# Optimization experiments

Hardware: AMD Instinct MI355X
Metric: run time of the kernel (lower is better)

The kernel has to match this reference:

```python
import jax, jax.numpy as jnp
import numpy as np

N = 50000          # nodes
E = 800000         # edges
IN_F = 128         # in_features
C = 1.0            # curvature (all learnable curvatures init to 1.0)
GIN_EPS = 0.0      # LorentzGIN eps
EPS = 1e-7
NUM_CLASSES = 10


def arcosh(x):
    x = jnp.maximum(x, 1.0 + EPS)
    return jnp.log(x + jnp.sqrt(x * x - 1.0))


def log_map_zero(y, c):
    # log map at hyperboloid origin (sqrt(c),0,...,0); tangent with first coord 0
    sc = np.sqrt(c).astype(np.float32)
    y0, tail = y[..., :1], y[..., 1:]
    dist = sc * arcosh(y0 / sc + EPS)                       # induced distance to origin
    nrm = jnp.sqrt(jnp.sum(tail * tail, axis=-1, keepdims=True) + EPS)
    return jnp.concatenate([jnp.zeros_like(y0), dist / nrm * tail], axis=-1)


def exp_map_zero(dp, c):
    # exp map at origin; dp tangent with first coord 0; re-normalized onto hyperboloid
    sc = np.sqrt(c).astype(np.float32)
    tail = dp[..., 1:]
    n = jnp.sqrt(jnp.clip(jnp.sum(tail * tail, axis=-1, keepdims=True) + EPS, 1e-6, None))
    n_cut = jnp.minimum(n, 50.0)
    tail_out = sc * jnp.sinh(n_cut / sc) * tail / n
    first = jnp.sqrt(c + jnp.sum(tail_out * tail_out, axis=-1, keepdims=True))
    return jnp.concatenate([first, tail_out], axis=-1)


def lorentz_linear(x, W, b, c):
    # matvec_regular: log-map, affine map on spatial coords, exp-map back
    xt = log_map_zero(x, c)                                  # first coord is 0
    mx = jnp.concatenate([xt[..., :1], xt[..., 1:] @ W.T + b], axis=-1)
    h = exp_map_zero(mx, c)
    cond = jnp.all(mx == 0, axis=-1, keepdims=True)
    return jnp.where(cond, 0.0, h)


def lorentz_act(x, c_in, c_out, act):
    xt = act(log_map_zero(x, c_in))
    xt = xt.at[..., 0].set(0.0)                              # normalize_tangent_zero
    return exp_map_zero(xt, c_out)


def forward(x, edge_index, W0, b0, W1, b1, W2, b2, Wc, bc):
    # LorentzGIN: tangent-space GIN aggregation (1+eps)*x_t + sum_{j in N(i)} x_t[j]
    xt = log_map_zero(x, C)
    agg = jax.ops.segment_sum(xt[edge_index[0]], edge_index[1], num_segments=N)
    out = (1.0 + GIN_EPS) * xt + agg
    out = out.at[..., 0].set(0.0)
    h = exp_map_zero(out, C)
    for (W, b) in ((W0, b0), (W1, b1), (W2, b2)):
        h = lorentz_act(lorentz_linear(h, W, b, C), C, C, jax.nn.relu)
    # manifold mean pooling over nodes
    ht = log_map_zero(h, C)                                  # [N, 384]
    hm = jnp.mean(ht, axis=0)                                # [384]
    hm = hm.at[0].set(0.0)                                   # normalize_tangent_zero
    h_classify = lorentz_linear(hm, Wc, bc, C)               # [NUM_CLASSES]
    prob = lorentz_act(h_classify, C, C, lambda t: jax.nn.softmax(t, axis=-1))
    return h_classify, prob


def setup_inputs():
    key = jax.random.key(0)
    ks = jax.random.split(key, 6)
    tail = 0.5 * jax.random.normal(ks[0], (N, IN_F - 1), jnp.float32)
    x0 = jnp.sqrt(C + jnp.sum(tail * tail, axis=-1, keepdims=True))
    x = jnp.concatenate([x0, tail], axis=-1)                 # points on the hyperboloid
    edge_index = jax.random.randint(ks[1], (2, E), 0, N)

    def lin(k, o, i):
        kw, kb = jax.random.split(k)
        s = 1.0 / np.sqrt(i)
        return (jax.random.uniform(kw, (o - 1, i - 1), jnp.float32, -s, s),
                jax.random.uniform(kb, (o - 1,), jnp.float32, -s, s))

    W0, b0 = lin(ks[2], 128, 128)
    W1, b1 = lin(ks[3], 256, 128)
    W2, b2 = lin(ks[4], 384, 256)
    Wc, bc = lin(ks[5], NUM_CLASSES, 384)
    return dict(x=x, edge_index=edge_index, W0=W0, b0=b0, W1=W1, b1=b1,
                W2=W2, b2=b2, Wc=Wc, bc=bc)


def reference(x, edge_index, W0, b0, W1, b1, W2, b2, Wc, bc):
    return forward(x, edge_index, W0, b0, W1, b1, W2, b2, Wc, bc)
```

## Files before the change

### kernel.cpp

```cpp
#include <hip/hip_runtime.h>
#include <math.h>

#define EPSF 1e-7f

typedef unsigned short ushort_t;
typedef __attribute__((ext_vector_type(8))) short bf16x8;
typedef __attribute__((ext_vector_type(4))) float f32x4;

__device__ __forceinline__ float fsinh(float x) { return 0.5f * (__expf(x) - __expf(-x)); }
__device__ __forceinline__ float arcosh_f(float x) {
    x = fmaxf(x, 1.0f + EPSF);
    return __logf(x + sqrtf(x * x - 1.0f));
}

__device__ __forceinline__ unsigned short f2bf(float f) {
    union { float f; unsigned u; } c; c.f = f;
    unsigned r = c.u + 0x7FFFu + ((c.u >> 16) & 1u);
    return (unsigned short)(r >> 16);
}
__device__ __forceinline__ float bf2f(unsigned short u) {
    union { unsigned u; float f; } c; c.u = ((unsigned)u) << 16;
    return c.f;
}

__device__ __forceinline__ float wredsum(float v) {
#pragma unroll
    for (int off = 32; off; off >>= 1) v += __shfl_xor(v, off, 64);
    return v;
}

__device__ __forceinline__ float ep_coef(float s1, float sp) {
    bool allz = (s1 == 0.0f);
    float n1 = sqrtf(fmaxf(s1 + EPSF, 1e-6f));
    float fac1 = fsinh(fminf(n1, 50.f)) / n1;
    float S2 = allz ? 0.f : fac1 * fac1 * s1;
    float first1 = allz ? 0.f : sqrtf(1.f + S2);
    float dist = arcosh_f(first1 + EPSF);
    float rs = dist / sqrtf(S2 + EPSF);
    float coef1 = allz ? 0.f : rs * fac1;
    float S3 = coef1 * coef1 * sp;
    float n2 = sqrtf(fmaxf(S3 + EPSF, 1e-6f));
    float fac2 = fsinh(fminf(n2, 50.f)) / n2;
    float S4 = fac2 * fac2 * S3;
    float first2 = sqrtf(1.f + S4);
    float dist2 = arcosh_f(first2 + EPSF);
    return dist2 / sqrtf(S4 + EPSF) * fac2 * coef1;
}

__device__ __forceinline__ void llds16(const void* g, void* l) {
    __builtin_amdgcn_global_load_lds((const __attribute__((address_space(1))) unsigned int*)g,
                                     (__attribute__((address_space(3))) unsigned int*)l,
                                     16, 0, 0);
}

__global__ __launch_bounds__(64) void k_log0(const float* __restrict__ x,
                                             char* __restrict__ Abase, int N) {
    int i = blockIdx.x, t = threadIdx.x;
    float2 v = *reinterpret_cast<const float2*>(x + (size_t)i * 128 + 2 * t);
    float y0 = __shfl(v.x, 0, 64);
    float a0 = (t == 0) ? 0.f : v.x;
    float s = wredsum(a0 * a0 + v.y * v.y);
    float dist = arcosh_f(y0 + EPSF);
    float scl = dist / sqrtf(s + EPSF);
    ushort2 o;
    o.x = f2bf(scl * a0);
    o.y = f2bf(scl * v.y);
    *reinterpret_cast<ushort2*>(Abase + (size_t)i * 512 + 256 + 4 * t) = o;
}

__global__ __launch_bounds__(256) void k_c1(const int* __restrict__ edst,
                                            int* __restrict__ gcnt,
                                            int E, int NBKT, int EPB) {
    __shared__ int cnt[64];
    int blk = blockIdx.x, t = threadIdx.x;
    for (int i = t; i < NBKT; i += 256) cnt[i] = 0;
    __syncthreads();
    int lo = blk * EPB, hi = min(lo + EPB, E);
    for (int e = lo + t; e < hi; e += 256) atomicAdd(&cnt[edst[e] >> 10], 1);
    __syncthreads();
    for (int i = t; i < NBKT; i += 256) gcnt[blk * NBKT + i] = cnt[i];
}

__global__ __launch_bounds__(64) void k_c2(int* __restrict__ gcnt,
                                           int* __restrict__ bstart, int NBLK, int NBKT) {
    __shared__ int sh[10816];
    __shared__ int tot[64];
    __shared__ int bs[65];
    int t = threadIdx.x;
    int total = NBLK * NBKT;
    for (int i = t; i < total; i += 64) sh[i] = gcnt[i];
    __syncthreads();
    if (t < NBKT) {
        int run = 0;
        for (int blk = 0; blk < NBLK; ++blk) {
            int idx = blk * NBKT + t;
            int c = sh[idx]; sh[idx] = run; run += c;
        }
        tot[t] = run;
    }
    __syncthreads();
    if (t == 0) {
        int r = 0;
        for (int b = 0; b < NBKT; ++b) { bs[b] = r; r += tot[b]; }
        bs[NBKT] = r;
    }
    __syncthreads();
    if (t < NBKT) {
        bstart[t] = bs[t];
        if (t == 0) bstart[NBKT] = bs[NBKT];
    }
    for (int i = t; i < total; i += 64) gcnt[i] = sh[i] + bs[i % NBKT];
}

__global__ __launch_bounds__(256) void k_c3(const int* __restrict__ esrc,
                                            const int* __restrict__ edst,
                                            const int* __restrict__ gcnt,
                                            int* __restrict__ ebuf,
                                            int E, int NBKT, int EPB) {
    __shared__ int cur[64];
    int blk = blockIdx.x, t = threadIdx.x;
    for (int i = t; i < NBKT; i += 256) cur[i] = 0;
    __syncthreads();
    int lo = blk * EPB, hi = min(lo + EPB, E);
    for (int e = lo + t; e < hi; e += 256) {
        int d = edst[e], s = esrc[e];
        int b = d >> 10;
        int r = atomicAdd(&cur[b], 1);
        ebuf[gcnt[blk * NBKT + b] + r] = ((d & 1023) << 17) | s;
    }
}

__global__ __launch_bounds__(1024) void k_c4(const int* __restrict__ ebuf,
                                             const int* __restrict__ bstart,
                                             int* __restrict__ row_ptr,
                                             int* __restrict__ srcl,
                                             int N, int NBKT, int E) {
    __shared__ int cnt[1024];
    __shared__ int cur[1024];
    __shared__ int wsum[17];
    int b = blockIdx.x, t = threadIdx.x;
    int lane = t & 63, wv = t >> 6;
    int lo = b << 10;
    int nn = min(1024, N - lo);
    cnt[t] = 0;
    __syncthreads();
    int es = bstart[b], ee = bstart[b + 1];
    for (int e = es + t; e < ee; e += 1024) atomicAdd(&cnt[ebuf[e] >> 17], 1);
    __syncthreads();
    int c = cnt[t];
    int sc = c;
#pragma unroll
    for (int off = 1; off < 64; off <<= 1) {
        int v = __shfl_up(sc, off, 64);
        if (lane >= off) sc += v;
    }
    if (lane == 63) wsum[wv + 1] = sc;
    if (t == 0) wsum[0] = 0;
    __syncthreads();
    if (t == 0) {
        for (int w = 1; w < 16; ++w) wsum[w + 1] += wsum[w];
    }
    __syncthreads();
    int rp = es + wsum[wv] + sc - c;
    cur[t] = rp;
    if (t < nn) row_ptr[lo + t] = rp;
    if (b == NBKT - 1 && t == 0) row_ptr[N] = E;
    __syncthreads();
    for (int e = es + t; e < ee; e += 1024) {
        int p = ebuf[e];
        int r = atomicAdd(&cur[p >> 17], 1);
        srcl[r] = p & 0x1FFFF;
    }
}

__global__ __launch_bounds__(64) void k_agg(const char* __restrict__ Abase,
                                            const int* __restrict__ row_ptr,
                                            const int* __restrict__ srcl,
                                            ushort_t* __restrict__ Ab, int N) {
    int i = blockIdx.x, t = threadIdx.x;
    const char* base = Abase + 256 + 4 * t;
    ushort2 sv = *reinterpret_cast<const ushort2*>(base + (size_t)i * 512);
    float p0[8], p1[8];
    p0[0] = bf2f(sv.x); p1[0] = bf2f(sv.y);
#pragma unroll
    for (int q = 1; q < 8; ++q) { p0[q] = 0.f; p1[q] = 0.f; }
    int b = row_ptr[i], e = row_ptr[i + 1];
    int k = b;
    for (; k + 8 <= e; k += 8) {
        int s[8];
#pragma unroll
        for (int q = 0; q < 8; ++q) s[q] = srcl[k + q];
        ushort2 v[8];
#pragma unroll
        for (int q = 0; q < 8; ++q)
            v[q] = *reinterpret_cast<const ushort2*>(base + (size_t)s[q] * 512);
#pragma unroll
        for (int q = 0; q < 8; ++q) { p0[q] += bf2f(v[q].x); p1[q] += bf2f(v[q].y); }
    }
    for (; k < e; ++k) {
        int s = srcl[k];
        ushort2 v = *reinterpret_cast<const ushort2*>(base + (size_t)s * 512);
        p0[0] += bf2f(v.x); p1[0] += bf2f(v.y);
    }
    float u0 = ((p0[0] + p0[1]) + (p0[2] + p0[3])) + ((p0[4] + p0[5]) + (p0[6] + p0[7]));
    float u1 = ((p1[0] + p1[1]) + (p1[2] + p1[3])) + ((p1[4] + p1[5]) + (p1[6] + p1[7]));
    if (t == 0) u0 = 0.f;
    float s1 = wredsum(u0 * u0 + u1 * u1);
    float n = sqrtf(fmaxf(s1 + EPSF, 1e-6f));
    float fac = fsinh(fminf(n, 50.f)) / n;
    float S2 = fac * fac * s1;
    float first = sqrtf(1.f + S2);
    float dist = arcosh_f(first + EPSF);
    float C = dist / sqrtf(S2 + EPSF) * fac;
    ushort2 o;
    o.x = f2bf(C * u0);
    o.y = f2bf(C * u1);
    *reinterpret_cast<ushort2*>(Ab + (size_t)i * 256 + 2 * t) = o;
}

__global__ void k_convw3(const float* __restrict__ W0, const float* __restrict__ W1,
                         const float* __restrict__ W2,
                         ushort_t* __restrict__ Wb0, ushort_t* __restrict__ Wb1,
                         ushort_t* __restrict__ Wb2,
                         int o1, int i1, int Kp1, int o2, int i2, int Kp2,
                         int o3, int i3, int Kp3, int t1, int t2, int t3) {
    int idx = blockIdx.x * blockDim.x + threadIdx.x;
    const float* W; ushort_t* Wb; int ncols, K, Kp, shift;
    if (idx < t1) { W = W0; Wb = Wb0; ncols = o1; K = i1; Kp = Kp1; shift = 1; }
    else if (idx < t1 + t2) { idx -= t1; W = W1; Wb = Wb1; ncols = o2; K = i2; Kp = Kp2; shift = 0; }
    else if (idx < t1 + t2 + t3) { idx -= t1 + t2; W = W2; Wb = Wb2; ncols = o3; K = i3; Kp = Kp3; shift = 0; }
    else return;
    int o = idx / Kp, kk = idx - o * Kp;
    int ks = kk - shift;
    float v = 0.f;
    if (o < ncols && ks >= 0 && ks < K) v = W[(size_t)o * K + ks];
    Wb[idx] = f2bf(v);
}

__global__ __launch_bounds__(256) void k_gemm(const ushort_t* __restrict__ Ab, int lda,
                                              const ushort_t* __restrict__ Wb, int ldw,
                                              const float* __restrict__ bias,
                                              ushort_t* __restrict__ Yb, int ldy,
                                              int Kp, int ncols) {
    __shared__ ushort_t As[128 * 32];
    __shared__ ushort_t Bs[128 * 32];
    int tid = threadIdx.x;
    int lane = tid & 63, wv = tid >> 6;
    int bm = blockIdx.x * 128, bn = blockIdx.y * 128;
    int r = lane & 15, g4 = lane >> 4;
    int wr = (wv >> 1) * 64, wc = (wv & 1) * 64;

    f32x4 acc[4][4] = {};
    for (int k0 = 0; k0 < Kp; k0 += 32) {
#pragma unroll
        for (int ci = 0; ci < 2; ++ci) {
            int L = (wv * 2 + ci) * 1024 + lane * 16;
            int row = L >> 6, kb = L & 63;
            const char* ga = (const char*)Ab + ((size_t)(bm + row) * lda + k0) * 2 + kb;
            llds16(ga, (char*)As + (wv * 2 + ci) * 1024);
            const char* gb = (const char*)Wb + ((size_t)(bn + row) * ldw + k0) * 2 + kb;
            llds16(gb, (char*)Bs + (wv * 2 + ci) * 1024);
        }
        __syncthreads();
        bf16x8 af[4], bfr[4];
#pragma unroll
        for (int m = 0; m < 4; ++m)
            af[m] = *reinterpret_cast<const bf16x8*>((const char*)As + (wr + m * 16 + r) * 64 + g4 * 16);
#pragma unroll
        for (int n2 = 0; n2 < 4; ++n2)
            bfr[n2] = *reinterpret_cast<const bf16x8*>((const char*)Bs + (wc + n2 * 16 + r) * 64 + g4 * 16);
#pragma unroll
        for (int m = 0; m < 4; ++m)
#pragma unroll
            for (int n2 = 0; n2 < 4; ++n2)
                acc[m][n2] = __builtin_amdgcn_mfma_f32_16x16x32_bf16(af[m], bfr[n2], acc[m][n2], 0, 0, 0);
        __syncthreads();
    }
#pragma unroll
    for (int n2 = 0; n2 < 4; ++n2) {
        int col = bn + wc + n2 * 16 + r;
        if (col >= ncols) continue;
        float bv = bias[col];
#pragma unroll
        for (int m = 0; m < 4; ++m) {
#pragma unroll
            for (int j = 0; j < 4; ++j) {
                int row = bm + wr + m * 16 + g4 * 4 + j;
                Yb[(size_t)row * ldy + col] = f2bf(acc[m][n2][j] + bv);
            }
        }
    }
}

__global__ __launch_bounds__(256) void k_gemmf(const ushort_t* __restrict__ Ab, int lda,
                                               const ushort_t* __restrict__ Wb, int ldw,
                                               const float* __restrict__ bias,
                                               ushort_t* __restrict__ Out,
                                               int Kp, int ncols) {
    __shared__ ushort_t As[128 * 32];
    __shared__ ushort_t Bs[128 * 32];
    __shared__ float s1buf[2][128];
    __shared__ float spbuf[2][128];
    __shared__ float Cbuf[128];
    int tid = threadIdx.x;
    int lane = tid & 63, wv = tid >> 6;
    int bm = blockIdx.x * 128;
    int r = lane & 15, g4 = lane >> 4;
    int wr = (wv >> 1) * 64, wc = (wv & 1) * 64;
    int half = wv & 1;

    f32x4 acc[4][4] = {};
    for (int k0 = 0; k0 < Kp; k0 += 32) {
#pragma unroll
        for (int ci = 0; ci < 2; ++ci) {
            int L = (wv * 2 + ci) * 1024 + lane * 16;
            int row = L >> 6, kb = L & 63;
            const char* ga = (const char*)Ab + ((size_t)(bm + row) * lda + k0) * 2 + kb;
            llds16(ga, (char*)As + (wv * 2 + ci) * 1024);
            const char* gb = (const char*)Wb + ((size_t)(row) * ldw + k0) * 2 + kb;
            llds16(gb, (char*)Bs + (wv * 2 + ci) * 1024);
        }
        __syncthreads();
        bf16x8 af[4], bfr[4];
#pragma unroll
        for (int m = 0; m < 4; ++m)
            af[m] = *reinterpret_cast<const bf16x8*>((const char*)As + (wr + m * 16 + r) * 64 + g4 * 16);
#pragma unroll
        for (int n2 = 0; n2 < 4; ++n2)
            bfr[n2] = *reinterpret_cast<const bf16x8*>((const char*)Bs + (wc + n2 * 16 + r) * 64 + g4 * 16);
#pragma unroll
        for (int m = 0; m < 4; ++m)
#pragma unroll
            for (int n2 = 0; n2 < 4; ++n2)
                acc[m][n2] = __builtin_amdgcn_mfma_f32_16x16x32_bf16(af[m], bfr[n2], acc[m][n2], 0, 0, 0);
        __syncthreads();
    }
    float bv[4];
#pragma unroll
    for (int n2 = 0; n2 < 4; ++n2) {
        int col = wc + n2 * 16 + r;
        bv[n2] = (col < ncols) ? bias[col] : 0.f;
    }
#pragma unroll
    for (int m = 0; m < 4; ++m) {
#pragma unroll
        for (int j = 0; j < 4; ++j) {
            float s1l = 0.f, spl = 0.f;
#pragma unroll
            for (int n2 = 0; n2 < 4; ++n2) {
                int col = wc + n2 * 16 + r;
                float y = (col < ncols) ? (acc[m][n2][j] + bv[n2]) : 0.f;
                acc[m][n2][j] = y;
                s1l += y * y;
                float ym = fmaxf(y, 0.f);
                spl += ym * ym;
            }
#pragma unroll
            for (int off = 1; off < 16; off <<= 1) {
                s1l += __shfl_xor(s1l, off, 64);
                spl += __shfl_xor(spl, off, 64);
            }
            if (r == 0) {
                int row = wr + m * 16 + g4 * 4 + j;
                s1buf[half][row] = s1l;
                spbuf[half][row] = spl;
            }
        }
    }
    __syncthreads();
    if (tid < 128) {
        float s1 = s1buf[0][tid] + s1buf[1][tid];
        float sp = spbuf[0][tid] + spbuf[1][tid];
        Cbuf[tid] = ep_coef(s1, sp);
    }
    __syncthreads();
#pragma unroll
    for (int m = 0; m < 4; ++m) {
#pragma unroll
        for (int j = 0; j < 4; ++j) {
            int rloc = wr + m * 16 + g4 * 4 + j;
            float C = Cbuf[rloc];
            size_t rowoff = (size_t)(bm + rloc) * 256;
#pragma unroll
            for (int n2 = 0; n2 < 4; ++n2) {
                int col = wc + n2 * 16 + r;
                Out[rowoff + col] = f2bf(C * fmaxf(acc[m][n2][j], 0.f));
            }
        }
    }
}

template <int NCP>
__global__ __launch_bounds__(64) void k_ep(const ushort_t* __restrict__ Y, int ldy,
                                           ushort_t* __restrict__ out, int ldo, int N) {
    constexpr int CH = NCP / 128;
    int i = blockIdx.x, t = threadIdx.x;
    const ushort_t* yr = Y + (size_t)i * ldy;
    float y[2 * CH], ym[2 * CH];
#pragma unroll
    for (int c = 0; c < CH; ++c) {
        ushort2 v = *reinterpret_cast<const ushort2*>(yr + c * 128 + 2 * t);
        y[2 * c] = bf2f(v.x);
        y[2 * c + 1] = bf2f(v.y);
    }
    if (t == 63) y[2 * CH - 1] = 0.f;
    float s1l = 0.f, spl = 0.f;
#pragma unroll
    for (int q = 0; q < 2 * CH; ++q) {
        s1l += y[q] * y[q];
        ym[q] = fmaxf(y[q], 0.f);
        spl += ym[q] * ym[q];
    }
#pragma unroll
    for (int off = 32; off; off >>= 1) {
        s1l += __shfl_xor(s1l, off, 64);
        spl += __shfl_xor(spl, off, 64);
    }
    float C = ep_coef(s1l, spl);
    ushort_t* orow = out + (size_t)i * ldo;
#pragma unroll
    for (int c = 0; c < CH; ++c) {
        ushort2 o;
        o.x = f2bf(C * ym[2 * c]);
        o.y = f2bf(C * ym[2 * c + 1]);
        *reinterpret_cast<ushort2*>(orow + c * 128 + 2 * t) = o;
    }
}

__global__ __launch_bounds__(64) void k_coef(const ushort_t* __restrict__ Y, int ldy,
                                             float* __restrict__ coef, int N) {
    constexpr int CH = 3;
    int i = blockIdx.x, t = threadIdx.x;
    const ushort_t* yr = Y + (size_t)i * ldy;
    float y[2 * CH];
#pragma unroll
    for (int c = 0; c < CH; ++c) {
        ushort2 v = *reinterpret_cast<const ushort2*>(yr + c * 128 + 2 * t);
        y[2 * c] = bf2f(v.x);
        y[2 * c + 1] = bf2f(v.y);
    }
    if (t == 63) y[2 * CH - 1] = 0.f;
    float s1l = 0.f, spl = 0.f;
#pragma unroll
    for (int q = 0; q < 2 * CH; ++q) {
        s1l += y[q] * y[q];
        float m = fmaxf(y[q], 0.f);
        spl += m * m;
    }
#pragma unroll
    for (int off = 32; off; off >>= 1) {
        s1l += __shfl_xor(s1l, off, 64);
        spl += __shfl_xor(spl, off, 64);
    }
    float C = ep_coef(s1l, spl);
    if (t == 0) coef[i] = C;
}

__global__ __launch_bounds__(192) void k_mean(const ushort_t* __restrict__ Y,
                                              const float* __restrict__ coef,
                                              float* __restrict__ partials, int N, int chunk) {
    int b = blockIdx.x;
    int t = threadIdx.x;
    int lo = b * chunk;
    int hi = lo + chunk; if (hi > N) hi = N;
    bool lastpair = (t == 191);
    float a0 = 0.f, a1 = 0.f;
    const ushort_t* p = Y + (size_t)lo * 384 + 2 * t;
    for (int n = lo; n < hi; ++n, p += 384) {
        float c = coef[n];
        ushort2 v = *reinterpret_cast<const ushort2*>(p);
        a0 += c * fmaxf(bf2f(v.x), 0.f);
        if (!lastpair) a1 += c * fmaxf(bf2f(v.y), 0.f);
    }
    float* orow = partials + (size_t)b * 384;
    orow[2 * t] = a0;
    orow[2 * t + 1] = a1;
}

__global__ __launch_bounds__(256) void k_mred(const float* __restrict__ partials,
                                              float* __restrict__ hm, int nparts, int N) {
    __shared__ float sb[256];
    int j = blockIdx.x, t = threadIdx.x;
    float v = 0.f;
    for (int p = t; p < nparts; p += 256) v += partials[(size_t)p * 384 + j];
    sb[t] = v; __syncthreads();
    for (int st = 128; st > 0; st >>= 1) { if (t < st) sb[t] += sb[t + st]; __syncthreads(); }
    if (t == 0) hm[j] = sb[0] / (float)N;
}

__global__ __launch_bounds__(64) void k_head(const float* __restrict__ hm,
                                             const float* __restrict__ Wc,
                                             const float* __restrict__ bc,
                                             float* __restrict__ dout, int ic, int oc) {
    int t = threadIdx.x;
    float h[6];
    float ss = 0.f;
#pragma unroll
    for (int c = 0; c < 6; ++c) {
        int j = t + 64 * c;
        h[c] = (j < ic) ? hm[j] : 0.f;
        ss += h[c] * h[c];
    }
    float ssum = wredsum(ss);
    float dist = logf(1.0f + EPSF + sqrtf((1.0f + EPSF) * (1.0f + EPSF) - 1.0f));
    float scl = dist / sqrtf(ssum + EPSF);
    float mxv[9];
#pragma unroll
    for (int o = 0; o < 9; ++o) {
        float p = 0.f;
        if (o < oc) {
#pragma unroll
            for (int c = 0; c < 6; ++c) {
                int j = t + 64 * c;
                if (j < ic) p += h[c] * Wc[(size_t)o * ic + j];
            }
        }
        float s = wredsum(p);
        mxv[o] = (o < oc) ? (scl * s + bc[o]) : 0.f;
    }
    if (t == 0) {
        float y[10], tt[10], lt[11], p[11], t3[11];
        float s1 = 0.f, sab = 0.f;
        for (int j = 0; j < 9; ++j) {
            y[j] = (j < oc) ? mxv[j] : 0.f;
            s1 += y[j] * y[j]; sab += fabsf(y[j]);
        }
        bool allz = (sab == 0.f);
        float n = sqrtf(fmaxf(s1 + EPSF, 1e-6f));
        float sh = sinhf(fminf(n, 50.f));
        float s2 = 0.f;
        for (int j = 0; j < oc; ++j) { tt[j] = allz ? 0.f : sh * y[j] / n; s2 += tt[j] * tt[j]; }
        float first = allz ? 0.f : sqrtf(1.f + s2);
        dout[0] = first;
        for (int j = 0; j < oc; ++j) dout[1 + j] = tt[j];
        float xx = fmaxf(first + EPSF, 1.0f + EPSF);
        float dist2 = logf(xx + sqrtf(xx * xx - 1.0f));
        float nrm2 = sqrtf(s2 + EPSF);
        lt[0] = 0.f;
        for (int j = 0; j < oc; ++j) lt[1 + j] = dist2 / nrm2 * tt[j];
        float m = lt[0];
        for (int j = 1; j <= oc; ++j) m = fmaxf(m, lt[j]);
        float es = 0.f;
        for (int j = 0; j <= oc; ++j) { p[j] = expf(lt[j] - m); es += p[j]; }
        for (int j = 0; j <= oc; ++j) p[j] /= es;
        p[0] = 0.f;
        float s3 = 0.f;
        for (int j = 1; j <= oc; ++j) s3 += p[j] * p[j];
        float n3 = sqrtf(fmaxf(s3 + EPSF, 1e-6f));
        float sh3 = sinhf(fminf(n3, 50.f));
        float s4 = 0.f;
        for (int j = 1; j <= oc; ++j) { t3[j] = sh3 * p[j] / n3; s4 += t3[j] * t3[j]; }
        dout[1 + oc] = sqrtf(1.f + s4);
        for (int j = 1; j <= oc; ++j) dout[1 + oc + j] = t3[j];
    }
}

extern "C" void kernel_launch(void* const* d_in, const int* in_sizes, int n_in,
                              void* d_out, int out_size, void* d_ws, size_t ws_size,
                              hipStream_t stream) {
    if (n_in < 10) return;
    const float* x   = (const float*)d_in[0];
    const int*   ei  = (const int*)d_in[1];
    const float* W0  = (const float*)d_in[2];
    const float* b0  = (const float*)d_in[3];
    const float* W1  = (const float*)d_in[4];
    const float* b1  = (const float*)d_in[5];
    const float* W2  = (const float*)d_in[6];
    const float* b2  = (const float*)d_in[7];
    const float* Wc  = (const float*)d_in[8];
    const float* bc  = (const float*)d_in[9];
    float* dout = (float*)d_out;

    int N = in_sizes[0] / 128;
    int E = in_sizes[1] / 2;
    int o1 = in_sizes[3];
    int i1 = in_sizes[2] / o1;
    int o2 = in_sizes[5];
    int i2 = in_sizes[4] / o2;
    int o3 = in_sizes[7];
    int i3 = in_sizes[6] / o3;
    int oc = in_sizes[9];
    int ic = in_sizes[8] / oc;

    int M_pad = ((N + 127) / 128) * 128;
    int Kp1 = ((i1 + 31) / 32) * 32;
    int Kp2 = ((i2 + 31) / 32) * 32;
    int Kp3 = ((i3 + 31) / 32) * 32;
    int Np1 = ((o1 + 127) / 128) * 128;
    int Np2 = ((o2 + 127) / 128) * 128;
    int Np3 = ((o3 + 127) / 128) * 128;

    const int* esrc = ei;
    const int* edst = ei + E;

    char* ws = (char*)d_ws;
    auto alloc = [&](size_t bytes) {
        char* p = ws;
        ws += (bytes + 511) & ~(size_t)511;
        return p;
    };
    ushort_t* Ab     = (ushort_t*)alloc((size_t)M_pad * 256 * 2);
    ushort_t* R      = (ushort_t*)alloc((size_t)M_pad * 384 * 2);
    ushort_t* Wb0    = (ushort_t*)alloc((size_t)Np1 * Kp1 * 2);
    ushort_t* Wb1    = (ushort_t*)alloc((size_t)Np2 * Kp2 * 2);
    ushort_t* Wb2    = (ushort_t*)alloc((size_t)Np3 * Kp3 * 2);
    int*      ebuf   = (int*)alloc((size_t)E * 4);
    int*      gcnt   = (int*)alloc((size_t)256 * 64 * 4);
    int*      bstart = (int*)alloc(128 * 4);
    int*      row_ptr= (int*)alloc((size_t)(N + 1) * 4);
    int*      srcl   = (int*)alloc((size_t)E * 4);
    float*    coefb  = (float*)alloc((size_t)N * 4);
    float*    partials = (float*)alloc((size_t)2048 * 384 * 4);
    float*    hmbuf  = (float*)alloc(512 * 4);
    (void)ws_size;

    int NBKT = (N + 1023) >> 10;
    int EPB = 4096;
    int NBLK_E = (E + EPB - 1) / EPB;

    int t1 = Np1 * Kp1, t2 = Np2 * Kp2, t3 = Np3 * Kp3;
    k_convw3<<<dim3((t1 + t2 + t3 + 255) / 256), dim3(256), 0, stream>>>(
        W0, W1, W2, Wb0, Wb1, Wb2, o1, i1, Kp1, o2, i2, Kp2, o3, i3, Kp3, t1, t2, t3);
    k_log0<<<dim3(N), dim3(64), 0, stream>>>(x, (char*)Ab, N);
    k_c1<<<dim3(NBLK_E), dim3(256), 0, stream>>>(edst, gcnt, E, NBKT, EPB);
    k_c2<<<dim3(1), dim3(64), 0, stream>>>(gcnt, bstart, NBLK_E, NBKT);
    k_c3<<<dim3(NBLK_E), dim3(256), 0, stream>>>(esrc, edst, gcnt, ebuf, E, NBKT, EPB);
    k_c4<<<dim3(NBKT), dim3(1024), 0, stream>>>(ebuf, bstart, row_ptr, srcl, N, NBKT, E);
    k_agg<<<dim3(N), dim3(64), 0, stream>>>((const char*)Ab, row_ptr, srcl, Ab, N);
    k_gemmf<<<dim3(M_pad / 128), dim3(256), 0, stream>>>(Ab, 256, Wb0, Kp1, b0, Ab, Kp1, o1);
    k_gemm<<<dim3(M_pad / 128, Np2 / 128), dim3(256), 0, stream>>>(Ab, 256, Wb1, Kp2, b1, R, 256, Kp2, o2);
    k_ep<256><<<dim3(N), dim3(64), 0, stream>>>(R, 256, Ab, 256, N);
    k_gemm<<<dim3(M_pad / 128, Np3 / 128), dim3(256), 0, stream>>>(Ab, 256, Wb2, Kp3, b2, R, 384, Kp3, o3);
    k_coef<<<dim3(N), dim3(64), 0, stream>>>(R, 384, coefb, N);
    int NBLK = 2048;
    int chunk = (N + NBLK - 1) / NBLK;
    k_mean<<<dim3(NBLK), dim3(192), 0, stream>>>(R, coefb, partials, N, chunk);
    k_mred<<<dim3(383), dim3(256), 0, stream>>>(partials, hmbuf, NBLK, N);
    k_head<<<dim3(1), dim3(64), 0, stream>>>(hmbuf, Wc, bc, dout, ic, oc);
}
```

Before: 245.1 us.

## Fuse row-norm epilogues into GEMMs and defer per-row scale to next GEMM

The separate per-row epilogue kernels (k_ep after GEMM2, k_coef after GEMM3) are removed. Each GEMM now writes per-column-block partial sums of y² and relu(y)² to small buffers, and a tiny k_cf kernel reduces them into a per-row coefficient. GEMM2 stores relu(y) unscaled, and GEMM3 applies the row coefficient to its accumulator before adding the bias, which is valid because the scale is linear per row. This removes full-matrix reads and writes of the intermediate activations, at the cost of extra partial buffers, two small launches and a separate Y3 buffer.

```diff
diff --git a/kernel.cpp b/kernel.cpp
--- a/kernel.cpp
+++ b/kernel.cpp
@@ -237,61 +237,6 @@
     Wb[idx] = f2bf(v);
 }
 
-__global__ __launch_bounds__(256) void k_gemm(const ushort_t* __restrict__ Ab, int lda,
-                                              const ushort_t* __restrict__ Wb, int ldw,
-                                              const float* __restrict__ bias,
-                                              ushort_t* __restrict__ Yb, int ldy,
-                                              int Kp, int ncols) {
-    __shared__ ushort_t As[128 * 32];
-    __shared__ ushort_t Bs[128 * 32];
-    int tid = threadIdx.x;
-    int lane = tid & 63, wv = tid >> 6;
-    int bm = blockIdx.x * 128, bn = blockIdx.y * 128;
-    int r = lane & 15, g4 = lane >> 4;
-    int wr = (wv >> 1) * 64, wc = (wv & 1) * 64;
-
-    f32x4 acc[4][4] = {};
-    for (int k0 = 0; k0 < Kp; k0 += 32) {
-#pragma unroll
-        for (int ci = 0; ci < 2; ++ci) {
-            int L = (wv * 2 + ci) * 1024 + lane * 16;
-            int row = L >> 6, kb = L & 63;
-            const char* ga = (const char*)Ab + ((size_t)(bm + row) * lda + k0) * 2 + kb;
-            llds16(ga, (char*)As + (wv * 2 + ci) * 1024);
-            const char* gb = (const char*)Wb + ((size_t)(bn + row) * ldw + k0) * 2 + kb;
-            llds16(gb, (char*)Bs + (wv * 2 + ci) * 1024);
-        }
-        __syncthreads();
-        bf16x8 af[4], bfr[4];
-#pragma unroll
-        for (int m = 0; m < 4; ++m)
-            af[m] = *reinterpret_cast<const bf16x8*>((const char*)As + (wr + m * 16 + r) * 64 + g4 * 16);
-#pragma unroll
-        for (int n2 = 0; n2 < 4; ++n2)
-            bfr[n2] = *reinterpret_cast<const bf16x8*>((const char*)Bs + (wc + n2 * 16 + r) * 64 + g4 * 16);
-#pragma unroll
-        for (int m = 0; m < 4; ++m)
-#pragma unroll
-            for (int n2 = 0; n2 < 4; ++n2)
-                acc[m][n2] = __builtin_amdgcn_mfma_f32_16x16x32_bf16(af[m], bfr[n2], acc[m][n2], 0, 0, 0);
-        __syncthreads();
-    }
-#pragma unroll
-    for (int n2 = 0; n2 < 4; ++n2) {
-        int col = bn + wc + n2 * 16 + r;
-        if (col >= ncols) continue;
-        float bv = bias[col];
-#pragma unroll
-        for (int m = 0; m < 4; ++m) {
-#pragma unroll
-            for (int j = 0; j < 4; ++j) {
-                int row = bm + wr + m * 16 + g4 * 4 + j;
-                Yb[(size_t)row * ldy + col] = f2bf(acc[m][n2][j] + bv);
-            }
-        }
-    }
-}
-
 __global__ __launch_bounds__(256) void k_gemmf(const ushort_t* __restrict__ Ab, int lda,
                                                const ushort_t* __restrict__ Wb, int ldw,
                                                const float* __restrict__ bias,
@@ -369,9 +314,7 @@
     }
     __syncthreads();
     if (tid < 128) {
-        float s1 = s1buf[0][tid] + s1buf[1][tid];
-        float sp = spbuf[0][tid] + spbuf[1][tid];
-        Cbuf[tid] = ep_coef(s1, sp);
+        Cbuf[tid] = ep_coef(s1buf[0][tid] + s1buf[1][tid], spbuf[0][tid] + spbuf[1][tid]);
     }
     __syncthreads();
 #pragma unroll
@@ -390,70 +333,186 @@
     }
 }
 
-template <int NCP>
-__global__ __launch_bounds__(64) void k_ep(const ushort_t* __restrict__ Y, int ldy,
-                                           ushort_t* __restrict__ out, int ldo, int N) {
-    constexpr int CH = NCP / 128;
-    int i = blockIdx.x, t = threadIdx.x;
-    const ushort_t* yr = Y + (size_t)i * ldy;
-    float y[2 * CH], ym[2 * CH];
-#pragma unroll
-    for (int c = 0; c < CH; ++c) {
-        ushort2 v = *reinterpret_cast<const ushort2*>(yr + c * 128 + 2 * t);
-        y[2 * c] = bf2f(v.x);
-        y[2 * c + 1] = bf2f(v.y);
-    }
-    if (t == 63) y[2 * CH - 1] = 0.f;
-    float s1l = 0.f, spl = 0.f;
-#pragma unroll
-    for (int q = 0; q < 2 * CH; ++q) {
-        s1l += y[q] * y[q];
-        ym[q] = fmaxf(y[q], 0.f);
-        spl += ym[q] * ym[q];
-    }
-#pragma unroll
-    for (int off = 32; off; off >>= 1) {
-        s1l += __shfl_xor(s1l, off, 64);
-        spl += __shfl_xor(spl, off, 64);
-    }
-    float C = ep_coef(s1l, spl);
-    ushort_t* orow = out + (size_t)i * ldo;
-#pragma unroll
-    for (int c = 0; c < CH; ++c) {
-        ushort2 o;
-        o.x = f2bf(C * ym[2 * c]);
-        o.y = f2bf(C * ym[2 * c + 1]);
-        *reinterpret_cast<ushort2*>(orow + c * 128 + 2 * t) = o;
-    }
-}
-
-__global__ __launch_bounds__(64) void k_coef(const ushort_t* __restrict__ Y, int ldy,
-                                             float* __restrict__ coef, int N) {
-    constexpr int CH = 3;
-    int i = blockIdx.x, t = threadIdx.x;
-    const ushort_t* yr = Y + (size_t)i * ldy;
-    float y[2 * CH];
-#pragma unroll
-    for (int c = 0; c < CH; ++c) {
-        ushort2 v = *reinterpret_cast<const ushort2*>(yr + c * 128 + 2 * t);
-        y[2 * c] = bf2f(v.x);
-        y[2 * c + 1] = bf2f(v.y);
-    }
-    if (t == 63) y[2 * CH - 1] = 0.f;
-    float s1l = 0.f, spl = 0.f;
-#pragma unroll
-    for (int q = 0; q < 2 * CH; ++q) {
-        s1l += y[q] * y[q];
-        float m = fmaxf(y[q], 0.f);
-        spl += m * m;
-    }
-#pragma unroll
-    for (int off = 32; off; off >>= 1) {
-        s1l += __shfl_xor(s1l, off, 64);
-        spl += __shfl_xor(spl, off, 64);
-    }
-    float C = ep_coef(s1l, spl);
-    if (t == 0) coef[i] = C;
+__global__ __launch_bounds__(256) void k_gemm2(const ushort_t* __restrict__ Ab, int lda,
+                                               const ushort_t* __restrict__ Wb, int ldw,
+                                               const float* __restrict__ bias,
+                                               ushort_t* __restrict__ Yb, int ldy,
+                                               float* __restrict__ pS1, float* __restrict__ pSp,
+                                               int NBY, int Kp, int ncols) {
+    __shared__ ushort_t As[128 * 32];
+    __shared__ ushort_t Bs[128 * 32];
+    __shared__ float s1buf[2][128];
+    __shared__ float spbuf[2][128];
+    int tid = threadIdx.x;
+    int lane = tid & 63, wv = tid >> 6;
+    int bm = blockIdx.x * 128, bn = blockIdx.y * 128, by = blockIdx.y;
+    int r = lane & 15, g4 = lane >> 4;
+    int wr = (wv >> 1) * 64, wc = (wv & 1) * 64;
+    int half = wv & 1;
+
+    f32x4 acc[4][4] = {};
+    for (int k0 = 0; k0 < Kp; k0 += 32) {
+#pragma unroll
+        for (int ci = 0; ci < 2; ++ci) {
+            int L = (wv * 2 + ci) * 1024 + lane * 16;
+            int row = L >> 6, kb = L & 63;
+            const char* ga = (const char*)Ab + ((size_t)(bm + row) * lda + k0) * 2 + kb;
+            llds16(ga, (char*)As + (wv * 2 + ci) * 1024);
+            const char* gb = (const char*)Wb + ((size_t)(bn + row) * ldw + k0) * 2 + kb;
+            llds16(gb, (char*)Bs + (wv * 2 + ci) * 1024);
+        }
+        __syncthreads();
+        bf16x8 af[4], bfr[4];
+#pragma unroll
+        for (int m = 0; m < 4; ++m)
+            af[m] = *reinterpret_cast<const bf16x8*>((const char*)As + (wr + m * 16 + r) * 64 + g4 * 16);
+#pragma unroll
+        for (int n2 = 0; n2 < 4; ++n2)
+            bfr[n2] = *reinterpret_cast<const bf16x8*>((const char*)Bs + (wc + n2 * 16 + r) * 64 + g4 * 16);
+#pragma unroll
+        for (int m = 0; m < 4; ++m)
+#pragma unroll
+            for (int n2 = 0; n2 < 4; ++n2)
+                acc[m][n2] = __builtin_amdgcn_mfma_f32_16x16x32_bf16(af[m], bfr[n2], acc[m][n2], 0, 0, 0);
+        __syncthreads();
+    }
+    float bv[4];
+#pragma unroll
+    for (int n2 = 0; n2 < 4; ++n2) {
+        int col = bn + wc + n2 * 16 + r;
+        bv[n2] = (col < ncols) ? bias[col] : 0.f;
+    }
+#pragma unroll
+    for (int m = 0; m < 4; ++m) {
+#pragma unroll
+        for (int j = 0; j < 4; ++j) {
+            int rloc = wr + m * 16 + g4 * 4 + j;
+            size_t rowoff = (size_t)(bm + rloc) * ldy;
+            float s1l = 0.f, spl = 0.f;
+#pragma unroll
+            for (int n2 = 0; n2 < 4; ++n2) {
+                int col = bn + wc + n2 * 16 + r;
+                float y = (col < ncols) ? (acc[m][n2][j] + bv[n2]) : 0.f;
+                float ym = fmaxf(y, 0.f);
+                s1l += y * y;
+                spl += ym * ym;
+                Yb[rowoff + col] = f2bf(ym);
+            }
+#pragma unroll
+            for (int off = 1; off < 16; off <<= 1) {
+                s1l += __shfl_xor(s1l, off, 64);
+                spl += __shfl_xor(spl, off, 64);
+            }
+            if (r == 0) {
+                s1buf[half][rloc] = s1l;
+                spbuf[half][rloc] = spl;
+            }
+        }
+    }
+    __syncthreads();
+    if (tid < 128) {
+        int row = bm + tid;
+        pS1[(size_t)row * NBY + by] = s1buf[0][tid] + s1buf[1][tid];
+        pSp[(size_t)row * NBY + by] = spbuf[0][tid] + spbuf[1][tid];
+    }
+}
+
+__global__ __launch_bounds__(256) void k_gemm3(const ushort_t* __restrict__ Ab, int lda,
+                                               const ushort_t* __restrict__ Wb, int ldw,
+                                               const float* __restrict__ bias,
+                                               const float* __restrict__ coef2,
+                                               ushort_t* __restrict__ Yb, int ldy,
+                                               float* __restrict__ pS1, float* __restrict__ pSp,
+                                               int NBY, int Kp, int ncols) {
+    __shared__ ushort_t As[128 * 32];
+    __shared__ ushort_t Bs[128 * 32];
+    __shared__ float s1buf[2][128];
+    __shared__ float spbuf[2][128];
+    int tid = threadIdx.x;
+    int lane = tid & 63, wv = tid >> 6;
+    int bm = blockIdx.x * 128, bn = blockIdx.y * 128, by = blockIdx.y;
+    int r = lane & 15, g4 = lane >> 4;
+    int wr = (wv >> 1) * 64, wc = (wv & 1) * 64;
+    int half = wv & 1;
+
+    f32x4 acc[4][4] = {};
+    for (int k0 = 0; k0 < Kp; k0 += 32) {
+#pragma unroll
+        for (int ci = 0; ci < 2; ++ci) {
+            int L = (wv * 2 + ci) * 1024 + lane * 16;
+            int row = L >> 6, kb = L & 63;
+            const char* ga = (const char*)Ab + ((size_t)(bm + row) * lda + k0) * 2 + kb;
+            llds16(ga, (char*)As + (wv * 2 + ci) * 1024);
+            const char* gb = (const char*)Wb + ((size_t)(bn + row) * ldw + k0) * 2 + kb;
+            llds16(gb, (char*)Bs + (wv * 2 + ci) * 1024);
+        }
+        __syncthreads();
+        bf16x8 af[4], bfr[4];
+#pragma unroll
+        for (int m = 0; m < 4; ++m)
+            af[m] = *reinterpret_cast<const bf16x8*>((const char*)As + (wr + m * 16 + r) * 64 + g4 * 16);
+#pragma unroll
+        for (int n2 = 0; n2 < 4; ++n2)
+            bfr[n2] = *reinterpret_cast<const bf16x8*>((const char*)Bs + (wc + n2 * 16 + r) * 64 + g4 * 16);
+#pragma unroll
+        for (int m = 0; m < 4; ++m)
+#pragma unroll
+            for (int n2 = 0; n2 < 4; ++n2)
+                acc[m][n2] = __builtin_amdgcn_mfma_f32_16x16x32_bf16(af[m], bfr[n2], acc[m][n2], 0, 0, 0);
+        __syncthreads();
+    }
+    float bv[4];
+#pragma unroll
+    for (int n2 = 0; n2 < 4; ++n2) {
+        int col = bn + wc + n2 * 16 + r;
+        bv[n2] = (col < ncols) ? bias[col] : 0.f;
+    }
+#pragma unroll
+    for (int m = 0; m < 4; ++m) {
+#pragma unroll
+        for (int j = 0; j < 4; ++j) {
+            int rloc = wr + m * 16 + g4 * 4 + j;
+            float c2 = coef2[bm + rloc];
+            size_t rowoff = (size_t)(bm + rloc) * ldy;
+            float s1l = 0.f, spl = 0.f;
+#pragma unroll
+            for (int n2 = 0; n2 < 4; ++n2) {
+                int col = bn + wc + n2 * 16 + r;
+                float y = (col < ncols) ? (c2 * acc[m][n2][j] + bv[n2]) : 0.f;
+                float ym = fmaxf(y, 0.f);
+                s1l += y * y;
+                spl += ym * ym;
+                Yb[rowoff + col] = f2bf(y);
+            }
+#pragma unroll
+            for (int off = 1; off < 16; off <<= 1) {
+                s1l += __shfl_xor(s1l, off, 64);
+                spl += __shfl_xor(spl, off, 64);
+            }
+            if (r == 0) {
+                s1buf[half][rloc] = s1l;
+                spbuf[half][rloc] = spl;
+            }
+        }
+    }
+    __syncthreads();
+    if (tid < 128) {
+        int row = bm + tid;
+        pS1[(size_t)row * NBY + by] = s1buf[0][tid] + s1buf[1][tid];
+        pSp[(size_t)row * NBY + by] = spbuf[0][tid] + spbuf[1][tid];
+    }
+}
+
+template <int P>
+__global__ __launch_bounds__(256) void k_cf(const float* __restrict__ pS1,
+                                            const float* __restrict__ pSp,
+                                            float* __restrict__ coef, int M) {
+    int i = blockIdx.x * 256 + threadIdx.x;
+    if (i >= M) return;
+    float s1 = 0.f, sp = 0.f;
+#pragma unroll
+    for (int p = 0; p < P; ++p) { s1 += pS1[(size_t)i * P + p]; sp += pSp[(size_t)i * P + p]; }
+    coef[i] = ep_coef(s1, sp);
 }
 
 __global__ __launch_bounds__(192) void k_mean(const ushort_t* __restrict__ Y,
@@ -586,9 +645,9 @@
     int Kp1 = ((i1 + 31) / 32) * 32;
     int Kp2 = ((i2 + 31) / 32) * 32;
     int Kp3 = ((i3 + 31) / 32) * 32;
-    int Np1 = ((o1 + 127) / 128) * 128;
     int Np2 = ((o2 + 127) / 128) * 128;
     int Np3 = ((o3 + 127) / 128) * 128;
+    int Np1 = 128;
 
     const int* esrc = ei;
     const int* edst = ei + E;
@@ -600,7 +659,8 @@
         return p;
     };
     ushort_t* Ab     = (ushort_t*)alloc((size_t)M_pad * 256 * 2);
-    ushort_t* R      = (ushort_t*)alloc((size_t)M_pad * 384 * 2);
+    ushort_t* R      = (ushort_t*)alloc((size_t)M_pad * 256 * 2);
+    ushort_t* Y3     = (ushort_t*)alloc((size_t)M_pad * 384 * 2);
     ushort_t* Wb0    = (ushort_t*)alloc((size_t)Np1 * Kp1 * 2);
     ushort_t* Wb1    = (ushort_t*)alloc((size_t)Np2 * Kp2 * 2);
     ushort_t* Wb2    = (ushort_t*)alloc((size_t)Np3 * Kp3 * 2);
@@ -609,7 +669,12 @@
     int*      bstart = (int*)alloc(128 * 4);
     int*      row_ptr= (int*)alloc((size_t)(N + 1) * 4);
     int*      srcl   = (int*)alloc((size_t)E * 4);
-    float*    coefb  = (float*)alloc((size_t)N * 4);
+    float*    pS1_2  = (float*)alloc((size_t)M_pad * 2 * 4);
+    float*    pSp_2  = (float*)alloc((size_t)M_pad * 2 * 4);
+    float*    pS1_3  = (float*)alloc((size_t)M_pad * 3 * 4);
+    float*    pSp_3  = (float*)alloc((size_t)M_pad * 3 * 4);
+    float*    coef2  = (float*)alloc((size_t)M_pad * 4);
+    float*    coef3  = (float*)alloc((size_t)M_pad * 4);
     float*    partials = (float*)alloc((size_t)2048 * 384 * 4);
     float*    hmbuf  = (float*)alloc(512 * 4);
     (void)ws_size;
@@ -628,13 +693,15 @@
     k_c4<<<dim3(NBKT), dim3(1024), 0, stream>>>(ebuf, bstart, row_ptr, srcl, N, NBKT, E);
     k_agg<<<dim3(N), dim3(64), 0, stream>>>((const char*)Ab, row_ptr, srcl, Ab, N);
     k_gemmf<<<dim3(M_pad / 128), dim3(256), 0, stream>>>(Ab, 256, Wb0, Kp1, b0, Ab, Kp1, o1);
-    k_gemm<<<dim3(M_pad / 128, Np2 / 128), dim3(256), 0, stream>>>(Ab, 256, Wb1, Kp2, b1, R, 256, Kp2, o2);
-    k_ep<256><<<dim3(N), dim3(64), 0, stream>>>(R, 256, Ab, 256, N);
-    k_gemm<<<dim3(M_pad / 128, Np3 / 128), dim3(256), 0, stream>>>(Ab, 256, Wb2, Kp3, b2, R, 384, Kp3, o3);
-    k_coef<<<dim3(N), dim3(64), 0, stream>>>(R, 384, coefb, N);
+    k_gemm2<<<dim3(M_pad / 128, Np2 / 128), dim3(256), 0, stream>>>(
+        Ab, 256, Wb1, Kp2, b1, R, 256, pS1_2, pSp_2, Np2 / 128, Kp2, o2);
+    k_cf<2><<<dim3((M_pad + 255) / 256), dim3(256), 0, stream>>>(pS1_2, pSp_2, coef2, M_pad);
+    k_gemm3<<<dim3(M_pad / 128, Np3 / 128), dim3(256), 0, stream>>>(
+        R, 256, Wb2, Kp3, b2, coef2, Y3, 384, pS1_3, pSp_3, Np3 / 128, Kp3, o3);
+    k_cf<3><<<dim3((M_pad + 255) / 256), dim3(256), 0, stream>>>(pS1_3, pSp_3, coef3, M_pad);
     int NBLK = 2048;
     int chunk = (N + NBLK - 1) / NBLK;
-    k_mean<<<dim3(NBLK), dim3(192), 0, stream>>>(R, coefb, partials, N, chunk);
+    k_mean<<<dim3(NBLK), dim3(192), 0, stream>>>(Y3, coef3, partials, N, chunk);
     k_mred<<<dim3(383), dim3(256), 0, stream>>>(partials, hmbuf, NBLK, N);
     k_head<<<dim3(1), dim3(64), 0, stream>>>(hmbuf, Wc, bc, dout, ic, oc);
 }
```

After: 214.0 us, median of 2. 1.15x faster.
